# Optimization experiments

Measured on AMD Instinct MI355X. Metric: run time of the kernel, lower is better.

## Reference

```python
import jax, jax.numpy as jnp
import numpy as np

N_NODES = 100000


def setup_inputs() -> dict:
    key = jax.random.key(0)
    k1, k2, k3, k4, k5 = jax.random.split(key, 5)
    E = 3200000
    F_IN, F_OUT = 128, 128
    x = jax.random.normal(k1, (N_NODES, F_IN), dtype=jnp.float32)
    row = jax.random.randint(k2, (E,), 0, N_NODES, dtype=jnp.int32)
    col = jax.random.randint(k3, (E,), 0, N_NODES, dtype=jnp.int32)
    # normalized-adjacency-like positive values
    edge_vals = jax.random.uniform(k4, (E,), dtype=jnp.float32)
    # xavier_uniform for W, zeros for bias (reset_parameters)
    limit = float(np.sqrt(6.0 / (F_IN + F_OUT)))
    W = jax.random.uniform(k5, (F_IN, F_OUT), dtype=jnp.float32, minval=-limit, maxval=limit)
    b = jnp.zeros((F_OUT,), dtype=jnp.float32)
    return {"x": x, "row": row, "col": col, "edge_vals": edge_vals, "W": W, "b": b}


def reference(x, row, col, edge_vals, W, b):
    # SpMM: (A @ x) where A is COO (row, col, edge_vals) of shape [N, N]
    gathered = edge_vals[:, None] * x[col]            # [E, F_in] irregular gather
    ax = jax.ops.segment_sum(gathered, row, num_segments=N_NODES)  # [N, F_in]
    # dense GEMM + bias
    return ax @ W + b
```

## Files before the change

kernel.cpp:

```cpp
#include <hip/hip_runtime.h>


#define FDIM 128
#define RPB   64
#define NBMAX 2048
#define MAXB  2560
#define TILE  4096

typedef __attribute__((ext_vector_type(8))) short short8;
typedef __attribute__((ext_vector_type(4))) float f32x4;

__device__ __forceinline__ unsigned bf16rn(float f) {
    unsigned u = __float_as_uint(f);
    return (u + 0x7FFFu + ((u >> 16) & 1u)) >> 16;
}

__global__ __launch_bounds__(256) void fat_gemm_binA(
        const float* __restrict__ x, const float* __restrict__ W,
        char* __restrict__ xwq, float* __restrict__ sglob,
        const int* __restrict__ row, const int* __restrict__ col,
        const float* __restrict__ ev,
        int* __restrict__ bucketcur, unsigned long long* __restrict__ bentry,
        int N, int E, int nb, int G1, int G2) {
    __shared__ char smem[32768];
    const int tid = threadIdx.x;
    const int bid = blockIdx.x;

    if (bid < G1) {
        for (int i = tid; i < 16384; i += 256) {
            int k = i >> 7, c = i & 127;
            ushort hv = (ushort)bf16rn(W[i]);
            int byteoff = c * 256 + ((k * 2) ^ ((c & 7) << 4));
            *(ushort*)(smem + byteoff) = hv;
        }
        __syncthreads();

        const int w = tid >> 6, l = tid & 63;
        const int g = l >> 4, c = l & 15;
        const int rbase = bid * 64 + w * 16;
        const int arow = rbase + c;
        const int kgrp = g * 8;

        f32x4 acc[8];
#pragma unroll
        for (int nt = 0; nt < 8; ++nt) acc[nt] = (f32x4){0.f, 0.f, 0.f, 0.f};

#pragma unroll
        for (int kb = 0; kb < 4; ++kb) {
            short8 a;
            if (arow < N) {
                const float* xp = x + (size_t)arow * FDIM + kb * 32 + kgrp;
                float4 x0 = ((const float4*)xp)[0];
                float4 x1 = ((const float4*)xp)[1];
                a[0] = (short)bf16rn(x0.x); a[1] = (short)bf16rn(x0.y);
                a[2] = (short)bf16rn(x0.z); a[3] = (short)bf16rn(x0.w);
                a[4] = (short)bf16rn(x1.x); a[5] = (short)bf16rn(x1.y);
                a[6] = (short)bf16rn(x1.z); a[7] = (short)bf16rn(x1.w);
            } else {
#pragma unroll
                for (int j = 0; j < 8; ++j) a[j] = 0;
            }
            const int kbyte = kb * 64 + g * 16;
#pragma unroll
            for (int nt = 0; nt < 8; ++nt) {
                int cc = nt * 16 + c;
                short8 bfrag = *(const short8*)(smem + cc * 256 + (kbyte ^ ((cc & 7) << 4)));
                acc[nt] = __builtin_amdgcn_mfma_f32_16x16x32_bf16(a, bfrag, acc[nt], 0, 0, 0);
            }
        }

        __syncthreads();

        float sr[4], inv[4];
#pragma unroll
        for (int r = 0; r < 4; ++r) {
            float m = 0.f;
#pragma unroll
            for (int nt = 0; nt < 8; ++nt) m = fmaxf(m, fabsf(acc[nt][r]));
#pragma unroll
            for (int mk = 1; mk < 16; mk <<= 1) m = fmaxf(m, __shfl_xor(m, mk));
            sr[r]  = m * (1.0f / 127.0f);
            inv[r] = (m > 0.f) ? (127.0f / m) : 0.f;
        }
        if (c == 0) {
#pragma unroll
            for (int r = 0; r < 4; ++r) {
                int gr = rbase + g * 4 + r;
                if (gr < N) sglob[gr] = sr[r];
            }
        }
        char* qlds = smem + w * 2048;
#pragma unroll
        for (int r = 0; r < 4; ++r)
#pragma unroll
            for (int nt = 0; nt < 8; ++nt) {
                int qi = (int)rintf(acc[nt][r] * inv[r]);
                qlds[(g * 4 + r) * 128 + nt * 16 + c] = (char)qi;
            }
        __syncthreads();

        uint4* dst = (uint4*)(xwq + (size_t)bid * 8192);
        const uint4* srcq = (const uint4*)smem;
#pragma unroll
        for (int t = 0; t < 2; ++t) {
            int i = t * 256 + tid;
            if (bid * 64 + (i >> 3) < N) dst[i] = srcq[i];
        }
    } else {
        int* tcnt  = (int*)smem;
        int* tbase = (int*)(smem + NBMAX * 4);

        for (long long t0 = (long long)(bid - G1) * TILE; t0 < E;
             t0 += (long long)G2 * TILE) {
            for (int i = tid; i < nb; i += 256) tcnt[i] = 0;
            __syncthreads();

            unsigned long long pk[16];
            int rr[16];
#pragma unroll
            for (int j = 0; j < 16; ++j) {
                long long e = t0 + j * 256 + tid;
                if (e < E) {
                    int r = row[e];
                    int cc = col[e];
                    unsigned evu = __float_as_uint(ev[e]);
                    pk[j] = ((unsigned long long)(unsigned)r << 47) |
                            ((unsigned long long)(unsigned)cc << 30) |
                            (unsigned long long)(evu >> 2);
                    rr[j] = r;
                    atomicAdd(&tcnt[r >> 6], 1);
                } else {
                    rr[j] = -1;
                }
            }
            __syncthreads();

            for (int i = tid; i < nb; i += 256) {
                int cc = tcnt[i];
                tbase[i] = cc ? atomicAdd(&bucketcur[i], cc) : 0;
                tcnt[i] = 0;
            }
            __syncthreads();

#pragma unroll
            for (int j = 0; j < 16; ++j) {
                if (rr[j] >= 0) {
                    int bk = rr[j] >> 6;
                    int pos = tbase[bk] + atomicAdd(&tcnt[bk], 1);
                    if (pos < MAXB) bentry[(size_t)bk * MAXB + pos] = pk[j];
                }
            }
            __syncthreads();
        }
    }
}

#define SBATCH(B)                                                               \
    {                                                                           \
        int2 p[B];                                                              \
        _Pragma("unroll") for (int j = 0; j < B; ++j) p[j] = sent[e + j];       \
        unsigned xv[B];                                                         \
        _Pragma("unroll") for (int j = 0; j < B; ++j)                           \
            xv[j] = *(const ushort*)(xwq + (unsigned)p[j].x + loff);            \
        _Pragma("unroll") for (int j = 0; j < B; ++j) {                         \
            float v = __int_as_float(p[j].y);                                   \
            float f0 = (float)(signed char)(xv[j] & 0xFF);                      \
            float f1 = (float)(signed char)(xv[j] >> 8);                        \
            if (j & 1) { a1.x = fmaf(v, f0, a1.x); a1.y = fmaf(v, f1, a1.y); }  \
            else       { a0.x = fmaf(v, f0, a0.x); a0.y = fmaf(v, f1, a0.y); }  \
        }                                                                       \
    }

__global__ __launch_bounds__(256) void sort_gather(
        const char* __restrict__ xwq, const float* __restrict__ sglob,
        const unsigned long long* __restrict__ bentry,
        const int* __restrict__ bucketcur,
        const float* __restrict__ bias, float* __restrict__ out, int N) {
    __shared__ int2 sent[MAXB];
    __shared__ int cnt[RPB];
    __shared__ int rs[RPB + 1];
    __shared__ int cur[RPB];
    const int tid = threadIdx.x;
    const int b = blockIdx.x;

    int sz = bucketcur[b];
    if (sz > MAXB) sz = MAXB;
    const unsigned long long* src = bentry + (size_t)b * MAXB;

    if (tid < RPB) cnt[tid] = 0;
    __syncthreads();

    unsigned long long pk[10];
    float sc[10];
#pragma unroll
    for (int k = 0; k < 10; ++k) {
        int i = tid + k * 256;
        if (i < sz) {
            unsigned long long p = src[i];
            pk[k] = p;
            atomicAdd(&cnt[(int)(p >> 47) & (RPB - 1)], 1);
            sc[k] = sglob[(unsigned)(p >> 30) & 0x1FFFFu];
        }
    }
    __syncthreads();

    if (tid < 64) {
        int v = cnt[tid];
        int s = v;
#pragma unroll
        for (int off = 1; off < 64; off <<= 1) {
            int t = __shfl_up(s, off);
            if (tid >= off) s += t;
        }
        rs[tid] = s - v;
        cur[tid] = s - v;
        if (tid == 63) rs[64] = s;
    }
    __syncthreads();

#pragma unroll
    for (int k = 0; k < 10; ++k) {
        int i = tid + k * 256;
        if (i < sz) {
            unsigned long long p = pk[k];
            int rib = (int)(p >> 47) & (RPB - 1);
            unsigned coff = (((unsigned)(p >> 30)) & 0x1FFFFu) << 7;
            float evf = __uint_as_float(((unsigned)p & 0x3FFFFFFFu) << 2);
            int pos = atomicAdd(&cur[rib], 1);
            sent[pos] = make_int2((int)coff, __float_as_int(evf * sc[k]));
        }
    }
    __syncthreads();

    const int lane = tid & 63;
    const int wid  = tid >> 6;
    const unsigned loff = (unsigned)(lane << 1);
    const float2 bias2 = *(const float2*)(bias + lane * 2);

    for (int rl = 0; rl < 16; ++rl) {
        const int rib = wid * 16 + rl;
        const int gr = b * RPB + rib;
        int e = rs[rib];
        const int end = rs[rib + 1];

        float2 a0 = bias2;
        float2 a1 = {0.f, 0.f};

        for (; e + 8 <= end; e += 8) SBATCH(8)
        if (e + 4 <= end) { SBATCH(4) e += 4; }
        for (; e < end; ++e) SBATCH(1)

        if (gr < N) {
            float2 o = {a0.x + a1.x, a0.y + a1.y};
            *(float2*)(out + (size_t)gr * FDIM + lane * 2) = o;
        }
    }
}

extern "C" void kernel_launch(void* const* d_in, const int* in_sizes, int n_in,
                              void* d_out, int out_size, void* d_ws, size_t ws_size,
                              hipStream_t stream) {
    const float* x   = (const float*)d_in[0];
    const int*   row = (const int*)d_in[1];
    const int*   col = (const int*)d_in[2];
    const float* ev  = (const float*)d_in[3];
    const float* W   = (const float*)d_in[4];
    const float* b   = (const float*)d_in[5];

    const int N = in_sizes[0] / FDIM;
    const int E = in_sizes[1];
    const int nb = (N + RPB - 1) / RPB;
    const int G1 = (N + 63) / 64;
    const int G2 = (E + TILE - 1) / TILE;

    char* ws = (char*)d_ws;
    char*     xwq       = (char*)(ws);
    float*    sglob     = (float*)(ws + 12800000);
    int*      bucketcur = (int*)(ws + 13200128);
    unsigned long long* bentry = (unsigned long long*)(ws + 13208320);
    float*    out       = (float*)d_out;

    hipMemsetAsync(bucketcur, 0, (size_t)nb * sizeof(int), stream);

    fat_gemm_binA<<<G1 + G2, 256, 0, stream>>>(x, W, xwq, sglob, row, col, ev,
                                               bucketcur, bentry, N, E, nb, G1, G2);
    sort_gather<<<nb, 256, 0, stream>>>(xwq, sglob, bentry, bucketcur, b, out, N);
}
```

Baseline: 150.4 us.

## Double rows per bucket and split wave into two halves gathering 4 bytes per lane

Row buckets grow from 64 to 128 rows, with matching changes to bucket capacity, binning shifts, per-thread entry registers and a two-chunk prefix scan. In the gather stage each wavefront is split into two 32-lane halves that process alternating edges. Each lane loads 4 int8 features instead of 2, and the halves are combined with a cross-lane shuffle at the end. The goal is wider loads, more independent gathers in flight and fewer blocks. The cost is more registers (18 packed entries per thread), larger shared memory, and a risk that the bucket capacity overflows.

```diff
diff --git a/kernel.cpp b/kernel.cpp
--- a/kernel.cpp
+++ b/kernel.cpp
@@ -2,9 +2,9 @@
 
 
 #define FDIM 128
-#define RPB   64
-#define NBMAX 2048
-#define MAXB  2560
+#define RPB   128
+#define NBMAX 1024
+#define MAXB  4608
 #define TILE  4096
 
 typedef __attribute__((ext_vector_type(8))) short short8;
@@ -128,7 +128,7 @@
                             ((unsigned long long)(unsigned)cc << 30) |
                             (unsigned long long)(evu >> 2);
                     rr[j] = r;
-                    atomicAdd(&tcnt[r >> 6], 1);
+                    atomicAdd(&tcnt[r >> 7], 1);
                 } else {
                     rr[j] = -1;
                 }
@@ -145,7 +145,7 @@
 #pragma unroll
             for (int j = 0; j < 16; ++j) {
                 if (rr[j] >= 0) {
-                    int bk = rr[j] >> 6;
+                    int bk = rr[j] >> 7;
                     int pos = tbase[bk] + atomicAdd(&tcnt[bk], 1);
                     if (pos < MAXB) bentry[(size_t)bk * MAXB + pos] = pk[j];
                 }
@@ -155,20 +155,27 @@
     }
 }
 
-#define SBATCH(B)                                                               \
-    {                                                                           \
-        int2 p[B];                                                              \
-        _Pragma("unroll") for (int j = 0; j < B; ++j) p[j] = sent[e + j];       \
-        unsigned xv[B];                                                         \
-        _Pragma("unroll") for (int j = 0; j < B; ++j)                           \
-            xv[j] = *(const ushort*)(xwq + (unsigned)p[j].x + loff);            \
-        _Pragma("unroll") for (int j = 0; j < B; ++j) {                         \
-            float v = __int_as_float(p[j].y);                                   \
-            float f0 = (float)(signed char)(xv[j] & 0xFF);                      \
-            float f1 = (float)(signed char)(xv[j] >> 8);                        \
-            if (j & 1) { a1.x = fmaf(v, f0, a1.x); a1.y = fmaf(v, f1, a1.y); }  \
-            else       { a0.x = fmaf(v, f0, a0.x); a0.y = fmaf(v, f1, a0.y); }  \
-        }                                                                       \
+#define PBATCH(B)                                                                \
+    {                                                                            \
+        int2 p[B];                                                               \
+        _Pragma("unroll") for (int j = 0; j < B; ++j) p[j] = sent[e + 2*j + h];  \
+        unsigned xv[B];                                                          \
+        _Pragma("unroll") for (int j = 0; j < B; ++j)                            \
+            xv[j] = *(const unsigned*)(xwq + (unsigned)p[j].x + loff);           \
+        _Pragma("unroll") for (int j = 0; j < B; ++j) {                          \
+            float v = __int_as_float(p[j].y);                                    \
+            float fx = (float)(signed char)(xv[j] & 0xFF);                       \
+            float fy = (float)(signed char)((xv[j] >> 8) & 0xFF);                \
+            float fz = (float)(signed char)((xv[j] >> 16) & 0xFF);               \
+            float fw = (float)(signed char)(xv[j] >> 24);                        \
+            if (j & 1) {                                                         \
+                a1.x = fmaf(v, fx, a1.x); a1.y = fmaf(v, fy, a1.y);              \
+                a1.z = fmaf(v, fz, a1.z); a1.w = fmaf(v, fw, a1.w);              \
+            } else {                                                             \
+                a0.x = fmaf(v, fx, a0.x); a0.y = fmaf(v, fy, a0.y);              \
+                a0.z = fmaf(v, fz, a0.z); a0.w = fmaf(v, fw, a0.w);              \
+            }                                                                    \
+        }                                                                        \
     }
 
 __global__ __launch_bounds__(256) void sort_gather(
@@ -190,10 +197,10 @@
     if (tid < RPB) cnt[tid] = 0;
     __syncthreads();
 
-    unsigned long long pk[10];
-    float sc[10];
-#pragma unroll
-    for (int k = 0; k < 10; ++k) {
+    unsigned long long pk[18];
+    float sc[18];
+#pragma unroll
+    for (int k = 0; k < 18; ++k) {
         int i = tid + k * 256;
         if (i < sz) {
             unsigned long long p = src[i];
@@ -205,21 +212,26 @@
     __syncthreads();
 
     if (tid < 64) {
-        int v = cnt[tid];
-        int s = v;
-#pragma unroll
-        for (int off = 1; off < 64; off <<= 1) {
-            int t = __shfl_up(s, off);
-            if (tid >= off) s += t;
-        }
-        rs[tid] = s - v;
-        cur[tid] = s - v;
-        if (tid == 63) rs[64] = s;
+        int carry = 0;
+#pragma unroll
+        for (int ch = 0; ch < 2; ++ch) {
+            int v = cnt[ch * 64 + tid];
+            int s = v;
+#pragma unroll
+            for (int off = 1; off < 64; off <<= 1) {
+                int t = __shfl_up(s, off);
+                if (tid >= off) s += t;
+            }
+            rs[ch * 64 + tid] = carry + s - v;
+            cur[ch * 64 + tid] = carry + s - v;
+            carry += __shfl(s, 63);
+        }
+        if (tid == 63) rs[RPB] = carry;
     }
     __syncthreads();
 
 #pragma unroll
-    for (int k = 0; k < 10; ++k) {
+    for (int k = 0; k < 18; ++k) {
         int i = tid + k * 256;
         if (i < sz) {
             unsigned long long p = pk[k];
@@ -234,26 +246,42 @@
 
     const int lane = tid & 63;
     const int wid  = tid >> 6;
-    const unsigned loff = (unsigned)(lane << 1);
-    const float2 bias2 = *(const float2*)(bias + lane * 2);
-
-    for (int rl = 0; rl < 16; ++rl) {
-        const int rib = wid * 16 + rl;
+    const int h    = lane >> 5;
+    const int s    = lane & 31;
+    const unsigned loff = (unsigned)(s << 2);
+    float4 bias4 = ((const float4*)bias)[s];
+    const float4 zero4 = {0.f, 0.f, 0.f, 0.f};
+
+    for (int rl = 0; rl < 32; ++rl) {
+        const int rib = wid * 32 + rl;
         const int gr = b * RPB + rib;
         int e = rs[rib];
         const int end = rs[rib + 1];
 
-        float2 a0 = bias2;
-        float2 a1 = {0.f, 0.f};
-
-        for (; e + 8 <= end; e += 8) SBATCH(8)
-        if (e + 4 <= end) { SBATCH(4) e += 4; }
-        for (; e < end; ++e) SBATCH(1)
-
-        if (gr < N) {
-            float2 o = {a0.x + a1.x, a0.y + a1.y};
-            *(float2*)(out + (size_t)gr * FDIM + lane * 2) = o;
-        }
+        float4 a0 = (h == 0) ? bias4 : zero4;
+        float4 a1 = zero4;
+
+        for (; e + 8 <= end; e += 8) PBATCH(4)
+        for (; e + 2 <= end; e += 2) PBATCH(1)
+        if (e < end) {
+            int2 p = sent[e];
+            unsigned xv = *(const unsigned*)(xwq + (unsigned)p.x + loff);
+            float v = (h == 0) ? __int_as_float(p.y) : 0.f;
+            a0.x = fmaf(v, (float)(signed char)(xv & 0xFF), a0.x);
+            a0.y = fmaf(v, (float)(signed char)((xv >> 8) & 0xFF), a0.y);
+            a0.z = fmaf(v, (float)(signed char)((xv >> 16) & 0xFF), a0.z);
+            a0.w = fmaf(v, (float)(signed char)(xv >> 24), a0.w);
+        }
+
+        float4 t;
+        t.x = a0.x + a1.x; t.y = a0.y + a1.y;
+        t.z = a0.z + a1.z; t.w = a0.w + a1.w;
+        t.x += __shfl_xor(t.x, 32);
+        t.y += __shfl_xor(t.y, 32);
+        t.z += __shfl_xor(t.z, 32);
+        t.w += __shfl_xor(t.w, 32);
+        if (h == 0 && gr < N)
+            *(float4*)(out + (size_t)gr * FDIM + s * 4) = t;
     }
 }
 
```

After: 168.9 us. 12.3% more time.
